# Kernel tuning notes

Hardware: AMD Instinct MI355X
Metric: run time of the kernel (lower is better)

## Reference

```python
import jax, jax.numpy as jnp
import numpy as np
from jax import lax

A = 20            # len(ANCHOR_RATIOS)=4 * len(ANCHOR_SCALES)=5 in neural-motifs config
TGT = 6           # anchor_target_dim
DIM = 512
IN_DIM = 1024
B, H, W = 16, 37, 37


def setup_inputs() -> dict:
    key = jax.random.key(0)
    k1, k2, k3, k4, k5 = jax.random.split(key, 5)
    fmap = jax.random.normal(k1, (B, IN_DIM, H, W), dtype=jnp.float32)
    # conv weights in OIHW, fan-in scaled init
    W1 = jax.random.normal(k2, (DIM, IN_DIM, 3, 3), dtype=jnp.float32) / np.sqrt(IN_DIM * 9)
    b1 = jnp.zeros((DIM,), dtype=jnp.float32)
    W2 = jax.random.normal(k3, (TGT * A, DIM, 1, 1), dtype=jnp.float32) / np.sqrt(DIM)
    b2 = jnp.zeros((TGT * A,), dtype=jnp.float32)
    return {"fmap": fmap, "W1": W1, "b1": b1, "W2": W2, "b2": b2}


def reference(fmap, W1, b1, W2, b2):
    dn = ("NCHW", "OIHW", "NCHW")
    # 3x3 conv, padding=1
    x = lax.conv_general_dilated(fmap, W1, window_strides=(1, 1), padding="SAME",
                                 dimension_numbers=dn) + b1[None, :, None, None]
    # ReLU6
    x = jnp.clip(x, 0.0, 6.0)
    # 1x1 conv -> [B, 6*A, H, W]
    x = lax.conv_general_dilated(x, W2, window_strides=(1, 1), padding="VALID",
                                 dimension_numbers=dn) + b2[None, :, None, None]
    # _reshape_channels: [B, C, H, W] -> [B, H, W, C], then split C -> (A, 6)
    b, c, h, w = x.shape
    x = jnp.transpose(x, (0, 2, 3, 1))
    return x.reshape(b, h, w, A, TGT)
```

## Files before the change

### kernel.cpp

```cpp
#include <hip/hip_runtime.h>
#include <stdint.h>

#define HW   1369
#define QW   39
#define QP   1616
#define QT   1536
#define CIN  1024
#define CMID 512
#define KTOT 9216
#define NTIL 144
#define SLOT 28672

typedef float  f32x4  __attribute__((ext_vector_type(4)));
typedef __bf16 bf16x8 __attribute__((ext_vector_type(8)));

__device__ __forceinline__ uint16_t f2bf(float f) {
  uint32_t u = __float_as_uint(f);
  u += 0x7fffu + ((u >> 16) & 1u);
  return (uint16_t)(u >> 16);
}

__device__ __forceinline__ void gll16(const void* g, void* l) {
  const __attribute__((address_space(1))) uint32_t* ga =
      (const __attribute__((address_space(1))) uint32_t*)(uintptr_t)g;
  __attribute__((address_space(3))) uint32_t* la =
      (__attribute__((address_space(3))) uint32_t*)(uint32_t)(uintptr_t)l;
  __builtin_amdgcn_global_load_lds(ga, la, 16, 0, 0);
}

__global__ void k_pad_transpose(const float* __restrict__ fmap, uint16_t* __restrict__ Xp) {
  __shared__ float t[32][33];
  const int b = blockIdx.z;
  const int c0 = blockIdx.y * 32;
  const int p0 = blockIdx.x * 32;
  const int tx = threadIdx.x, ty = threadIdx.y;
  const float* src = fmap + ((size_t)b * CIN + c0) * HW + p0;
#pragma unroll
  for (int i = 0; i < 4; ++i) {
    int cc = ty + i * 8;
    t[cc][tx] = (p0 + tx < HW) ? src[(size_t)cc * HW + tx] : 0.f;
  }
  __syncthreads();
#pragma unroll
  for (int i = 0; i < 4; ++i) {
    int pl = ty + i * 8;
    int p = p0 + pl;
    if (p < HW) {
      int h = p / 37, w = p - h * 37;
      int q = (h + 1) * QW + (w + 1);
      Xp[((size_t)b * QP + q) * CIN + c0 + tx] = f2bf(t[tx][pl]);
    }
  }
}

__global__ void k_pack_w1(const float* __restrict__ W1, uint16_t* __restrict__ Apk) {
  int idx = blockIdx.x * 256 + threadIdx.x;
  if (idx >= 512 * KTOT) return;
  int o = idx / KTOT, k = idx - o * KTOT;
  int r = k >> 10, c = k & 1023;
  Apk[idx] = f2bf(W1[((size_t)o * CIN + c) * 9 + r]);
}

__global__ void k_pack_w2(const float* __restrict__ W2, uint16_t* __restrict__ W2p) {
  int idx = blockIdx.x * 256 + threadIdx.x;
  int j = idx >> 9, o = idx & 511;
  W2p[idx] = (j < 120) ? f2bf(W2[j * 512 + o]) : (uint16_t)0;
}

__global__ __launch_bounds__(512, 1) void k_conv1(
    const uint16_t* __restrict__ Xp, const uint16_t* __restrict__ Apk,
    const float* __restrict__ b1, uint16_t* __restrict__ x1) {
  __shared__ __align__(16) uint16_t lds[2 * SLOT];

  const int tid  = threadIdx.x;
  const int wid  = tid >> 6, lane = tid & 63;
  const int lrow = lane & 15, lq = lane >> 4;
  const int wm   = wid >> 2,  wn = wid & 3;

  const int bid = blockIdx.x;
  const int g   = (bid & 7) * 32 + (bid >> 3);
  const int mt  = g >> 1, nt = g & 1;
  const int batch = mt >> 3, qb = (mt & 7) * 192;
  const int o0 = nt * 256;
  const uint16_t* Xb = Xp + (size_t)batch * QP * CIN;

  const int xorb    = (lrow & 7) << 4;
  const int col_el0 = ((lq * 16) ^ xorb) >> 1;
  const int col_el1 = col_el0 ^ 32;

  const int scol = ((tid & 7) ^ ((tid >> 3) & 7)) * 8;
  const int srow = tid >> 3;

  f32x4 acc[6][4] = {};

#define STAGE(u) do {                                                                 \
    if ((u) < NTIL) {                                                                 \
      const int cb_  = (u) / 9;                                                       \
      const int tap_ = (u) - cb_ * 9;                                                 \
      const int off_ = (tap_ / 3) * QW + tap_ % 3;                                    \
      const int c0_  = cb_ << 6;                                                      \
      uint16_t* sl = lds + ((u) & 1) * SLOT;                                          \
      _Pragma("unroll")                                                               \
      for (int j = 0; j < 3; ++j)                                                     \
        gll16(Xb + (size_t)(qb + off_ + j * 64 + srow) * CIN + c0_ + scol,            \
              sl + j * 4096 + wid * 512);                                             \
      _Pragma("unroll")                                                               \
      for (int j = 0; j < 4; ++j)                                                     \
        gll16(Apk + (size_t)(o0 + j * 64 + srow) * KTOT + (tap_ << 10) + c0_ + scol,  \
              sl + 12288 + j * 4096 + wid * 512);                                     \
    }                                                                                 \
  } while (0)

#define READF(kk) do {                                                                \
    const int ce = (kk) ? col_el1 : col_el0;                                          \
    _Pragma("unroll")                                                                 \
    for (int m = 0; m < 6; ++m)                                                       \
      av[m] = *(const bf16x8*)(As + (wm * 96 + m * 16 + lrow) * 64 + ce);             \
    _Pragma("unroll")                                                                 \
    for (int n = 0; n < 4; ++n)                                                       \
      bv[n] = *(const bf16x8*)(Bs + (wn * 64 + n * 16 + lrow) * 64 + ce);             \
  } while (0)

#define MFMA24 do {                                                                   \
    __builtin_amdgcn_s_setprio(1);                                                    \
    _Pragma("unroll")                                                                 \
    for (int m = 0; m < 6; ++m)                                                       \
      _Pragma("unroll")                                                               \
      for (int n = 0; n < 4; ++n)                                                     \
        acc[m][n] = __builtin_amdgcn_mfma_f32_16x16x32_bf16(                          \
            av[m], bv[n], acc[m][n], 0, 0, 0);                                        \
    __builtin_amdgcn_s_setprio(0);                                                    \
  } while (0)

  STAGE(0);
  STAGE(1);

  for (int t = 0; t < NTIL; ++t) {
    const uint16_t* As = lds + (t & 1) * SLOT;
    const uint16_t* Bs = As + 12288;
    if (t >= NTIL - 1) asm volatile("s_waitcnt vmcnt(0)" ::: "memory");
    else               asm volatile("s_waitcnt vmcnt(7)" ::: "memory");
    asm volatile("s_barrier" ::: "memory");
    __builtin_amdgcn_sched_barrier(0);
    bf16x8 av[6], bv[4];
    READF(0);
    MFMA24;
    READF(1);
    asm volatile("s_waitcnt lgkmcnt(0)" ::: "memory");
    __builtin_amdgcn_sched_barrier(0);
    asm volatile("s_barrier" ::: "memory");
    __builtin_amdgcn_sched_barrier(0);
    STAGE(t + 2);
    MFMA24;
  }

  const int qr = lq * 4;
#pragma unroll
  for (int n = 0; n < 4; ++n) {
    const int o = o0 + wn * 64 + n * 16 + lrow;
    const float bias = b1[o];
#pragma unroll
    for (int m = 0; m < 6; ++m) {
#pragma unroll
      for (int v = 0; v < 4; ++v) {
        const int q = qb + wm * 96 + m * 16 + qr + v;
        float x = acc[m][n][v] + bias;
        x = fminf(fmaxf(x, 0.f), 6.f);
        x1[((size_t)batch * QT + q) * CMID + o] = f2bf(x);
      }
    }
  }
#undef MFMA24
#undef READF
#undef STAGE
}

__global__ __launch_bounds__(256, 2) void k_conv2(
    const uint16_t* __restrict__ x1, const uint16_t* __restrict__ W2p,
    const float* __restrict__ b2, float* __restrict__ out) {
  __shared__ __align__(16) uint16_t lA[128 * 64];
  __shared__ __align__(16) uint16_t lB[128 * 64];
  const int tid = threadIdx.x;
  const int wid = tid >> 6, lane = tid & 63;
  const int b = blockIdx.z, q0 = blockIdx.x * 128;
  const uint16_t* Ab = x1 + (size_t)b * QT * CMID;
  const int wm = wid >> 1, wn = wid & 1;
  const int lrow = lane & 15, lk = (lane >> 4) * 8;
  f32x4 acc[4][4] = {};

  for (int kt = 0; kt < 8; ++kt) {
    const int c0 = kt << 6;
#pragma unroll
    for (int i = 0; i < 4; ++i) {
      int wb = i * 256 + wid * 64;
      int chunk = wb + lane;
      int row = chunk >> 3, ch = chunk & 7;
      gll16(Ab + (size_t)(q0 + row) * CMID + c0 + ch * 8, lA + wb * 8);
      gll16(W2p + (size_t)row * CMID + c0 + ch * 8, lB + wb * 8);
    }
    __syncthreads();
#pragma unroll
    for (int kk = 0; kk < 2; ++kk) {
      bf16x8 av[4], bv[4];
#pragma unroll
      for (int mi = 0; mi < 4; ++mi)
        av[mi] = *(const bf16x8*)(lA + (wm * 64 + mi * 16 + lrow) * 64 + kk * 32 + lk);
#pragma unroll
      for (int ni = 0; ni < 4; ++ni)
        bv[ni] = *(const bf16x8*)(lB + (wn * 64 + ni * 16 + lrow) * 64 + kk * 32 + lk);
#pragma unroll
      for (int mi = 0; mi < 4; ++mi)
#pragma unroll
        for (int ni = 0; ni < 4; ++ni)
          acc[mi][ni] = __builtin_amdgcn_mfma_f32_16x16x32_bf16(av[mi], bv[ni], acc[mi][ni], 0, 0, 0);
    }
    __syncthreads();
  }

  const int qr = (lane >> 4) * 4;
#pragma unroll
  for (int ni = 0; ni < 4; ++ni) {
    int j = wn * 64 + ni * 16 + lrow;
    if (j < 120) {
      float bias = b2[j];
#pragma unroll
      for (int mi = 0; mi < 4; ++mi) {
#pragma unroll
        for (int v = 0; v < 4; ++v) {
          int q = q0 + wm * 64 + mi * 16 + qr + v;
          int h = q / QW, w = q - h * QW;
          if (h < 37 && w < 37) {
            out[((size_t)b * HW + h * 37 + w) * 120 + j] = acc[mi][ni][v] + bias;
          }
        }
      }
    }
  }
}

extern "C" void kernel_launch(void* const* d_in, const int* in_sizes, int n_in,
                              void* d_out, int out_size, void* d_ws, size_t ws_size,
                              hipStream_t stream) {
  const float* fmap = (const float*)d_in[0];
  const float* W1   = (const float*)d_in[1];
  const float* b1   = (const float*)d_in[2];
  const float* W2   = (const float*)d_in[3];
  const float* b2   = (const float*)d_in[4];
  float* out = (float*)d_out;

  uint8_t* ws = (uint8_t*)d_ws;
  const size_t XP_BYTES  = (size_t)16 * QP * CIN * 2;
  const size_t W1P_BYTES = (size_t)512 * KTOT * 2;
  const size_t W2P_BYTES = (size_t)128 * 512 * 2;
  uint16_t* Xp  = (uint16_t*)ws;
  uint16_t* Apk = (uint16_t*)(ws + XP_BYTES);
  uint16_t* W2p = (uint16_t*)(ws + XP_BYTES + W1P_BYTES);
  uint16_t* x1  = (uint16_t*)(ws + XP_BYTES + W1P_BYTES + W2P_BYTES);

  hipMemsetAsync(Xp, 0, XP_BYTES, stream);
  k_pad_transpose<<<dim3(43, 32, 16), dim3(32, 8), 0, stream>>>(fmap, Xp);
  k_pack_w1<<<dim3((512 * KTOT + 255) / 256), dim3(256), 0, stream>>>(W1, Apk);
  k_pack_w2<<<dim3(256), dim3(256), 0, stream>>>(W2, W2p);
  k_conv1<<<dim3(256), dim3(512), 0, stream>>>(Xp, Apk, b1, x1);
  k_conv2<<<dim3(12, 1, 16), dim3(256), 0, stream>>>(x1, W2p, b2, out);
}
```

Measured before the change: 263.3 us.

## Load conv1 weight operand straight to registers and triple-buffer activation tiles in LDS

The 3x3 conv kernel no longer stages weight (B) tiles through LDS. Each wave loads its weight fragments with direct global loads into double-buffered registers, one tile ahead. Only the activation (A) tiles stay in LDS, now in a three-slot ring, and each tile needs one barrier instead of two. Launch bounds are raised to ask for two blocks per CU. This cuts LDS traffic and barrier stalls, but the register budget for two 512-thread blocks is tight against the 96 accumulators plus 64 prefetched B registers, so spills or lower occupancy are a risk. Weights are also re-fetched per wave from global or cache rather than shared through LDS.

```diff
diff --git a/kernel.cpp b/kernel.cpp
--- a/kernel.cpp
+++ b/kernel.cpp
@@ -9,7 +9,7 @@
 #define CMID 512
 #define KTOT 9216
 #define NTIL 144
-#define SLOT 28672
+#define ASLOT 12288
 
 typedef float  f32x4  __attribute__((ext_vector_type(4)));
 typedef __bf16 bf16x8 __attribute__((ext_vector_type(8)));
@@ -67,10 +67,10 @@
   W2p[idx] = (j < 120) ? f2bf(W2[j * 512 + o]) : (uint16_t)0;
 }
 
-__global__ __launch_bounds__(512, 1) void k_conv1(
+__global__ __launch_bounds__(512, 2) void k_conv1(
     const uint16_t* __restrict__ Xp, const uint16_t* __restrict__ Apk,
     const float* __restrict__ b1, uint16_t* __restrict__ x1) {
-  __shared__ __align__(16) uint16_t lds[2 * SLOT];
+  __shared__ __align__(16) uint16_t lds[3 * ASLOT];
 
   const int tid  = threadIdx.x;
   const int wid  = tid >> 6, lane = tid & 63;
@@ -91,68 +91,83 @@
   const int scol = ((tid & 7) ^ ((tid >> 3) & 7)) * 8;
   const int srow = tid >> 3;
 
+  const uint16_t* bp[4];
+#pragma unroll
+  for (int n = 0; n < 4; ++n)
+    bp[n] = Apk + (size_t)(o0 + wn * 64 + n * 16 + lrow) * KTOT + lq * 8;
+
   f32x4 acc[6][4] = {};
-
-#define STAGE(u) do {                                                                 \
+  bf16x8 bvA[8], bvB[8];
+
+#define STAGEA(u) do {                                                                \
     if ((u) < NTIL) {                                                                 \
       const int cb_  = (u) / 9;                                                       \
       const int tap_ = (u) - cb_ * 9;                                                 \
       const int off_ = (tap_ / 3) * QW + tap_ % 3;                                    \
       const int c0_  = cb_ << 6;                                                      \
-      uint16_t* sl = lds + ((u) & 1) * SLOT;                                          \
+      uint16_t* sl = lds + ((u) % 3) * ASLOT;                                         \
       _Pragma("unroll")                                                               \
       for (int j = 0; j < 3; ++j)                                                     \
         gll16(Xb + (size_t)(qb + off_ + j * 64 + srow) * CIN + c0_ + scol,            \
               sl + j * 4096 + wid * 512);                                             \
-      _Pragma("unroll")                                                               \
-      for (int j = 0; j < 4; ++j)                                                     \
-        gll16(Apk + (size_t)(o0 + j * 64 + srow) * KTOT + (tap_ << 10) + c0_ + scol,  \
-              sl + 12288 + j * 4096 + wid * 512);                                     \
     }                                                                                 \
   } while (0)
 
-#define READF(kk) do {                                                                \
-    const int ce = (kk) ? col_el1 : col_el0;                                          \
-    _Pragma("unroll")                                                                 \
-    for (int m = 0; m < 6; ++m)                                                       \
-      av[m] = *(const bf16x8*)(As + (wm * 96 + m * 16 + lrow) * 64 + ce);             \
-    _Pragma("unroll")                                                                 \
-    for (int n = 0; n < 4; ++n)                                                       \
-      bv[n] = *(const bf16x8*)(Bs + (wn * 64 + n * 16 + lrow) * 64 + ce);             \
+#define LOADB(u, BVL) do {                                                            \
+    const int cbn_  = (u) / 9;                                                        \
+    const int tapn_ = (u) - cbn_ * 9;                                                 \
+    const int eoff_ = (tapn_ << 10) + (cbn_ << 6);                                    \
+    _Pragma("unroll")                                                                 \
+    for (int n = 0; n < 4; ++n) {                                                     \
+      asm volatile("global_load_dwordx4 %0, %1, off"                                  \
+                   : "=v"(BVL[n]) : "v"(bp[n] + eoff_) : "memory");                   \
+      asm volatile("global_load_dwordx4 %0, %1, off"                                  \
+                   : "=v"(BVL[4 + n]) : "v"(bp[n] + eoff_ + 32) : "memory");          \
+    }                                                                                 \
   } while (0)
 
-#define MFMA24 do {                                                                   \
+#define TILE(t, BVU, BVL, LAST) do {                                                  \
+    if (LAST) asm volatile("s_waitcnt vmcnt(0)" ::: "memory");                        \
+    else      asm volatile("s_waitcnt vmcnt(3)" ::: "memory");                        \
+    asm volatile("s_barrier" ::: "memory");                                           \
+    __builtin_amdgcn_sched_barrier(0);                                                \
+    if (!(LAST)) { LOADB((t) + 1, BVL); STAGEA((t) + 2); }                            \
+    const uint16_t* As = lds + ((t) % 3) * ASLOT;                                     \
+    bf16x8 av[6];                                                                     \
+    _Pragma("unroll")                                                                 \
+    for (int m = 0; m < 6; ++m)                                                       \
+      av[m] = *(const bf16x8*)(As + (wm * 96 + m * 16 + lrow) * 64 + col_el0);        \
     __builtin_amdgcn_s_setprio(1);                                                    \
     _Pragma("unroll")                                                                 \
     for (int m = 0; m < 6; ++m)                                                       \
       _Pragma("unroll")                                                               \
       for (int n = 0; n < 4; ++n)                                                     \
         acc[m][n] = __builtin_amdgcn_mfma_f32_16x16x32_bf16(                          \
-            av[m], bv[n], acc[m][n], 0, 0, 0);                                        \
+            av[m], BVU[n], acc[m][n], 0, 0, 0);                                       \
+    __builtin_amdgcn_s_setprio(0);                                                    \
+    _Pragma("unroll")                                                                 \
+    for (int m = 0; m < 6; ++m)                                                       \
+      av[m] = *(const bf16x8*)(As + (wm * 96 + m * 16 + lrow) * 64 + col_el1);        \
+    __builtin_amdgcn_s_setprio(1);                                                    \
+    _Pragma("unroll")                                                                 \
+    for (int m = 0; m < 6; ++m)                                                       \
+      _Pragma("unroll")                                                               \
+      for (int n = 0; n < 4; ++n)                                                     \
+        acc[m][n] = __builtin_amdgcn_mfma_f32_16x16x32_bf16(                          \
+            av[m], BVU[4 + n], acc[m][n], 0, 0, 0);                                   \
     __builtin_amdgcn_s_setprio(0);                                                    \
   } while (0)
 
-  STAGE(0);
-  STAGE(1);
-
-  for (int t = 0; t < NTIL; ++t) {
-    const uint16_t* As = lds + (t & 1) * SLOT;
-    const uint16_t* Bs = As + 12288;
-    if (t >= NTIL - 1) asm volatile("s_waitcnt vmcnt(0)" ::: "memory");
-    else               asm volatile("s_waitcnt vmcnt(7)" ::: "memory");
-    asm volatile("s_barrier" ::: "memory");
-    __builtin_amdgcn_sched_barrier(0);
-    bf16x8 av[6], bv[4];
-    READF(0);
-    MFMA24;
-    READF(1);
-    asm volatile("s_waitcnt lgkmcnt(0)" ::: "memory");
-    __builtin_amdgcn_sched_barrier(0);
-    asm volatile("s_barrier" ::: "memory");
-    __builtin_amdgcn_sched_barrier(0);
-    STAGE(t + 2);
-    MFMA24;
-  }
+  LOADB(0, bvA);
+  STAGEA(0);
+  STAGEA(1);
+
+  for (int tp = 0; tp < NTIL - 2; tp += 2) {
+    TILE(tp,     bvA, bvB, false);
+    TILE(tp + 1, bvB, bvA, false);
+  }
+  TILE(NTIL - 2, bvA, bvB, false);
+  TILE(NTIL - 1, bvB, bvA, true);
 
   const int qr = lq * 4;
 #pragma unroll
@@ -170,9 +185,9 @@
       }
     }
   }
-#undef MFMA24
-#undef READF
-#undef STAGE
+#undef TILE
+#undef LOADB
+#undef STAGEA
 }
 
 __global__ __launch_bounds__(256, 2) void k_conv2(
```

New measurement: 404.3 us. 53.5% more time.

## Restructure conv1 main loop into four barrier-synchronized phases with single-tile prefetch

Applied to the files above, without the earlier changes.

The main GEMM loop of the 3x3 conv now issues the next tile's global-to-LDS load right after the wait, then splits each tile into four phases. Each phase reads half of the A fragments and, when needed, the B fragments, then runs 12 MFMAs between barriers. Prefetch depth drops from two tiles to one and every iteration waits on vmcnt(0). The aim is lower register pressure and tighter interleaving of LDS reads with MFMAs across waves. The cost is more barriers per iteration and less latency hiding for global loads.

```diff
diff --git a/kernel.cpp b/kernel.cpp
--- a/kernel.cpp
+++ b/kernel.cpp
@@ -111,47 +111,46 @@
     }                                                                                 \
   } while (0)
 
-#define READF(kk) do {                                                                \
-    const int ce = (kk) ? col_el1 : col_el0;                                          \
+#define PHASE(MH, KK, RDBV) do {                                                      \
+    const int ce = (KK) ? col_el1 : col_el0;                                          \
+    bf16x8 av[3];                                                                     \
+    if (RDBV) {                                                                       \
+      _Pragma("unroll")                                                               \
+      for (int n = 0; n < 4; ++n)                                                     \
+        bv[n] = *(const bf16x8*)(Bs + (wn * 64 + n * 16 + lrow) * 64 + ce);           \
+    }                                                                                 \
     _Pragma("unroll")                                                                 \
-    for (int m = 0; m < 6; ++m)                                                       \
-      av[m] = *(const bf16x8*)(As + (wm * 96 + m * 16 + lrow) * 64 + ce);             \
-    _Pragma("unroll")                                                                 \
-    for (int n = 0; n < 4; ++n)                                                       \
-      bv[n] = *(const bf16x8*)(Bs + (wn * 64 + n * 16 + lrow) * 64 + ce);             \
-  } while (0)
-
-#define MFMA24 do {                                                                   \
+    for (int m = 0; m < 3; ++m)                                                       \
+      av[m] = *(const bf16x8*)(As + (wm * 96 + (MH) * 48 + m * 16 + lrow) * 64 + ce); \
+    asm volatile("s_barrier" ::: "memory");                                           \
+    asm volatile("s_waitcnt lgkmcnt(0)" ::: "memory");                                \
+    __builtin_amdgcn_sched_barrier(0);                                                \
     __builtin_amdgcn_s_setprio(1);                                                    \
     _Pragma("unroll")                                                                 \
-    for (int m = 0; m < 6; ++m)                                                       \
+    for (int m = 0; m < 3; ++m)                                                       \
       _Pragma("unroll")                                                               \
       for (int n = 0; n < 4; ++n)                                                     \
-        acc[m][n] = __builtin_amdgcn_mfma_f32_16x16x32_bf16(                          \
-            av[m], bv[n], acc[m][n], 0, 0, 0);                                        \
+        acc[(MH) * 3 + m][n] = __builtin_amdgcn_mfma_f32_16x16x32_bf16(               \
+            av[m], bv[n], acc[(MH) * 3 + m][n], 0, 0, 0);                             \
     __builtin_amdgcn_s_setprio(0);                                                    \
+    asm volatile("s_barrier" ::: "memory");                                           \
+    __builtin_amdgcn_sched_barrier(0);                                                \
   } while (0)
 
   STAGE(0);
-  STAGE(1);
 
   for (int t = 0; t < NTIL; ++t) {
     const uint16_t* As = lds + (t & 1) * SLOT;
     const uint16_t* Bs = As + 12288;
-    if (t >= NTIL - 1) asm volatile("s_waitcnt vmcnt(0)" ::: "memory");
-    else               asm volatile("s_waitcnt vmcnt(7)" ::: "memory");
+    asm volatile("s_waitcnt vmcnt(0)" ::: "memory");
     asm volatile("s_barrier" ::: "memory");
     __builtin_amdgcn_sched_barrier(0);
-    bf16x8 av[6], bv[4];
-    READF(0);
-    MFMA24;
-    READF(1);
-    asm volatile("s_waitcnt lgkmcnt(0)" ::: "memory");
-    __builtin_amdgcn_sched_barrier(0);
-    asm volatile("s_barrier" ::: "memory");
-    __builtin_amdgcn_sched_barrier(0);
-    STAGE(t + 2);
-    MFMA24;
+    STAGE(t + 1);
+    bf16x8 bv[4];
+    PHASE(0, 0, 1);
+    PHASE(1, 0, 0);
+    PHASE(0, 1, 1);
+    PHASE(1, 1, 0);
   }
 
   const int qr = lq * 4;
@@ -170,8 +169,7 @@
       }
     }
   }
-#undef MFMA24
-#undef READF
+#undef PHASE
 #undef STAGE
 }
 
```

After: 283.6 us. 1.08x slower.
